# Optimization experiments

Measured on AMD Instinct MI355X. Metric: run time of the kernel, lower is better.

Reference implementation:

```python
import jax, jax.numpy as jnp
import numpy as np

N, C, S = 262144, 256, 16
BN_EPS = 1e-5


def setup_inputs() -> dict:
    key = jax.random.key(0)
    ks = jax.random.split(key, 8)
    x = jax.random.normal(ks[0], (N, C), dtype=jnp.float32)
    # strictly increasing cumulative offsets ending at N (guarantees nonzero counts)
    rng = np.random.default_rng(0)
    cuts = np.sort(rng.choice(np.arange(1, N), size=S - 1, replace=False))
    o = jnp.asarray(np.concatenate([cuts, [N]]), dtype=jnp.int64)
    # linear2_: Linear(C, C) (+ReLU, no BN in this branch)
    W2 = jax.random.normal(ks[1], (C, C), dtype=jnp.float32) / np.sqrt(C)
    b2 = jax.random.normal(ks[2], (C,), dtype=jnp.float32) * 0.01
    # linear1_: Linear(2C, C) + BatchNorm1d(C) + ReLU
    W1 = jax.random.normal(ks[3], (2 * C, C), dtype=jnp.float32) / np.sqrt(2 * C)
    b1 = jax.random.normal(ks[4], (C,), dtype=jnp.float32) * 0.01
    gamma = jnp.ones((C,), dtype=jnp.float32)
    beta = jnp.zeros((C,), dtype=jnp.float32)
    run_mean = jax.random.normal(ks[5], (C,), dtype=jnp.float32) * 0.01
    run_var = jnp.ones((C,), dtype=jnp.float32)
    return {"x": x, "o": o, "W2": W2, "b2": b2, "W1": W1, "b1": b1,
            "gamma": gamma, "beta": beta, "run_mean": run_mean, "run_var": run_var}


def reference(x, o, W2, b2, W1, b1, gamma, beta, run_mean, run_var):
    n, c = x.shape
    num_seg = o.shape[0]
    # segment id of each point: first offset strictly greater than index
    seg_ids = jnp.searchsorted(o, jnp.arange(n), side="right")  # [N]
    counts = jnp.diff(o, prepend=0).astype(x.dtype)             # [S]
    sums = jax.ops.segment_sum(x, seg_ids, num_segments=num_seg)  # [S, C]
    means = sums / counts[:, None]
    # linear2_ on per-segment mean, broadcast back to points
    h = jax.nn.relu(means @ W2 + b2)                            # [S, C]
    xc = jnp.concatenate([x, h[seg_ids]], axis=1)               # [N, 2C]
    # linear1_: Linear + BatchNorm1d (inference, running stats) + ReLU
    y = xc @ W1 + b1
    y = (y - run_mean) * jax.lax.rsqrt(run_var + BN_EPS) * gamma + beta
    return jax.nn.relu(y)
```

## Files before the change

### kernel.cpp

```cpp
#include <hip/hip_runtime.h>

#define C_DIM 256
#define S_SEG 16

typedef __attribute__((ext_vector_type(8))) short bf16x8;
typedef __attribute__((ext_vector_type(4))) float f32x4;

__device__ __forceinline__ short f2bf(float f) {
    unsigned u = __builtin_bit_cast(unsigned, f);
    u += 0x7FFF + ((u >> 16) & 1);
    return (short)(u >> 16);
}

__device__ __forceinline__ int o_get(const int* __restrict__ o_raw, int i) {
    return (o_raw[1] == 0) ? o_raw[2 * i] : o_raw[i];
}

__global__ __launch_bounds__(256) void k1_segsum(const float* __restrict__ x,
                                                 const int* __restrict__ o_raw,
                                                 float* __restrict__ sums) {
    __shared__ int o_s[S_SEG];
    __shared__ float4 partv[256];
    __shared__ int pseg[256];
    int t = threadIdx.x;
    if (t < S_SEG) o_s[t] = o_get(o_raw, t);
    __syncthreads();

    int rsub = t >> 6, cg = t & 63;
    int row0 = blockIdx.x * 256 + rsub * 64;
    const float4* xv = (const float4*)x;

    int cur = 0;
#pragma unroll
    for (int j = 0; j < S_SEG; ++j) cur += (row0 >= o_s[j]);
    int next = o_s[cur];

    float4 acc = make_float4(0.f, 0.f, 0.f, 0.f);
    for (int i = 0; i < 64; ++i) {
        int row = row0 + i;
        if (row >= next) {
            atomicAdd(&sums[cur * C_DIM + cg * 4 + 0], acc.x);
            atomicAdd(&sums[cur * C_DIM + cg * 4 + 1], acc.y);
            atomicAdd(&sums[cur * C_DIM + cg * 4 + 2], acc.z);
            atomicAdd(&sums[cur * C_DIM + cg * 4 + 3], acc.w);
            acc = make_float4(0.f, 0.f, 0.f, 0.f);
            do { cur++; next = o_s[cur]; } while (row >= next);
        }
        float4 v = xv[row * 64 + cg];
        acc.x += v.x; acc.y += v.y; acc.z += v.z; acc.w += v.w;
    }
    partv[t] = acc;
    pseg[t] = cur;
    __syncthreads();

    if (t < 64) {
        float4 a = partv[t];
        int s = pseg[t];
        for (int i = 1; i < 4; ++i) {
            int idx = i * 64 + t;
            int s2 = pseg[idx];
            float4 a2 = partv[idx];
            if (s2 == s) {
                a.x += a2.x; a.y += a2.y; a.z += a2.z; a.w += a2.w;
            } else {
                atomicAdd(&sums[s * C_DIM + t * 4 + 0], a.x);
                atomicAdd(&sums[s * C_DIM + t * 4 + 1], a.y);
                atomicAdd(&sums[s * C_DIM + t * 4 + 2], a.z);
                atomicAdd(&sums[s * C_DIM + t * 4 + 3], a.w);
                s = s2; a = a2;
            }
        }
        atomicAdd(&sums[s * C_DIM + t * 4 + 0], a.x);
        atomicAdd(&sums[s * C_DIM + t * 4 + 1], a.y);
        atomicAdd(&sums[s * C_DIM + t * 4 + 2], a.z);
        atomicAdd(&sums[s * C_DIM + t * 4 + 3], a.w);
    }
}

__global__ __launch_bounds__(256) void k2_small(const float* __restrict__ sums,
                                                const int* __restrict__ o_raw,
                                                const float* __restrict__ W2,
                                                const float* __restrict__ b2,
                                                const float* __restrict__ W1,
                                                const float* __restrict__ b1,
                                                const float* __restrict__ gamma,
                                                const float* __restrict__ beta,
                                                const float* __restrict__ rmean,
                                                const float* __restrict__ rvar,
                                                float* __restrict__ Cseg,
                                                short* __restrict__ W1s) {
    int t = threadIdx.x;
    int blk = blockIdx.x;
    if (blk < S_SEG) {
        __shared__ float mean_s[C_DIM];
        __shared__ float h_s[C_DIM];
        int s = blk;
        int lo = (s == 0) ? 0 : o_get(o_raw, s - 1);
        float inv = 1.0f / (float)(o_get(o_raw, s) - lo);
        mean_s[t] = sums[s * C_DIM + t] * inv;
        __syncthreads();
        float acc = b2[t];
#pragma unroll 4
        for (int k = 0; k < C_DIM; ++k) acc = fmaf(mean_s[k], W2[k * C_DIM + t], acc);
        h_s[t] = fmaxf(acc, 0.0f);
        __syncthreads();
        float acc2 = 0.f;
#pragma unroll 4
        for (int k = 0; k < C_DIM; ++k) acc2 = fmaf(h_s[k], W1[(C_DIM + k) * C_DIM + t], acc2);
        float sc = gamma[t] * rsqrtf(rvar[t] + 1e-5f);
        Cseg[s * C_DIM + t] = (b1[t] + acc2 - rmean[t]) * sc + beta[t];
    } else {
        int base = (blk - S_SEG) * 8192;
        for (int i = 0; i < 32; ++i) {
            int idx = base + i * 256 + t;
            int k = idx >> 8, c = idx & 255;
            float sc = gamma[c] * rsqrtf(rvar[c] + 1e-5f);
            float v = W1[k * C_DIM + c] * sc;
            int kb2 = k >> 5, q = (k >> 3) & 3, j = k & 7, nsub = c >> 4, r = c & 15;
            int off = ((kb2 * 16 + nsub) * 64 + q * 16 + r) * 8 + j;
            W1s[off] = f2bf(v);
        }
    }
}

__global__ __launch_bounds__(256) void k3_gemm(const float* __restrict__ x,
                                               const short* __restrict__ W1s,
                                               const float* __restrict__ Cseg,
                                               const int* __restrict__ o_raw,
                                               float* __restrict__ out) {
    __shared__ __align__(16) short As[2][4 * 2 * 64 * 8];
    __shared__ int o_s[S_SEG];

    int t = threadIdx.x;
    int wave = t >> 6, lane = t & 63;
    int q = lane >> 4, r = lane & 15;
    int wc = wave;
    int m0 = (int)(gridDim.x - 1 - blockIdx.x) * 64;

    if (t < S_SEG) o_s[t] = o_get(o_raw, t);

    f32x4 acc[4][4];
#pragma unroll
    for (int mt = 0; mt < 4; ++mt)
#pragma unroll
        for (int nt = 0; nt < 4; ++nt)
            acc[mt][nt] = (f32x4){0.f, 0.f, 0.f, 0.f};

    const float4* xv = (const float4*)x;
    int arow = t >> 3;
    int akc = t & 7;
    int kt_w = akc >> 2, q_w = akc & 3;
    int mt0 = arow >> 4, r0 = arow & 15;
    int slot0 = (mt0 * 2 + kt_w) * 64 + q_w * 16 + (r0 ^ q_w);
    int row1 = 32 + arow, mt1 = row1 >> 4, r1 = row1 & 15;
    int slot1 = (mt1 * 2 + kt_w) * 64 + q_w * 16 + (r1 ^ q_w);
    long gbase0 = (long)(m0 + arow) * 64 + akc * 2;
    long gbase1 = (long)(m0 + 32 + arow) * 64 + akc * 2;

    float4 c00, c01, c10, c11;
    c00 = xv[gbase0]; c01 = xv[gbase0 + 1];
    c10 = xv[gbase1]; c11 = xv[gbase1 + 1];
    {
        bf16x8 w0, w1;
        w0[0] = f2bf(c00.x); w0[1] = f2bf(c00.y); w0[2] = f2bf(c00.z); w0[3] = f2bf(c00.w);
        w0[4] = f2bf(c01.x); w0[5] = f2bf(c01.y); w0[6] = f2bf(c01.z); w0[7] = f2bf(c01.w);
        *(bf16x8*)&As[0][slot0 * 8] = w0;
        w1[0] = f2bf(c10.x); w1[1] = f2bf(c10.y); w1[2] = f2bf(c10.z); w1[3] = f2bf(c10.w);
        w1[4] = f2bf(c11.x); w1[5] = f2bf(c11.y); w1[6] = f2bf(c11.z); w1[7] = f2bf(c11.w);
        *(bf16x8*)&As[0][slot1 * 8] = w1;
    }
    __syncthreads();

    for (int kb = 0; kb < 4; ++kb) {
        if (kb < 3) {
            long o = (long)(kb + 1) * 16;
            c00 = xv[gbase0 + o]; c01 = xv[gbase0 + o + 1];
            c10 = xv[gbase1 + o]; c11 = xv[gbase1 + o + 1];
        }
        const short* Ab = As[kb & 1];
#pragma unroll
        for (int kt = 0; kt < 2; ++kt) {
            bf16x8 a[4], b[4];
#pragma unroll
            for (int mt = 0; mt < 4; ++mt)
                a[mt] = *(const bf16x8*)&Ab[((mt * 2 + kt) * 64 + q * 16 + (r ^ q)) * 8];
#pragma unroll
            for (int nt = 0; nt < 4; ++nt)
                b[nt] = *(const bf16x8*)&W1s[(((kb * 2 + kt) * 16 + wc * 4 + nt) * 64 + lane) * 8];
#pragma unroll
            for (int mt = 0; mt < 4; ++mt)
#pragma unroll
                for (int nt = 0; nt < 4; ++nt)
                    acc[mt][nt] = __builtin_amdgcn_mfma_f32_16x16x32_bf16(a[mt], b[nt], acc[mt][nt], 0, 0, 0);
        }
        if (kb < 3) {
            short* Aw = As[(kb + 1) & 1];
            bf16x8 w0, w1;
            w0[0] = f2bf(c00.x); w0[1] = f2bf(c00.y); w0[2] = f2bf(c00.z); w0[3] = f2bf(c00.w);
            w0[4] = f2bf(c01.x); w0[5] = f2bf(c01.y); w0[6] = f2bf(c01.z); w0[7] = f2bf(c01.w);
            *(bf16x8*)&Aw[slot0 * 8] = w0;
            w1[0] = f2bf(c10.x); w1[1] = f2bf(c10.y); w1[2] = f2bf(c10.z); w1[3] = f2bf(c10.w);
            w1[4] = f2bf(c11.x); w1[5] = f2bf(c11.y); w1[6] = f2bf(c11.z); w1[7] = f2bf(c11.w);
            *(bf16x8*)&Aw[slot1 * 8] = w1;
            __syncthreads();
        }
    }

#pragma unroll
    for (int mt = 0; mt < 4; ++mt) {
#pragma unroll
        for (int i = 0; i < 4; ++i) {
            int row = m0 + mt * 16 + q * 4 + i;
            int s = 0;
#pragma unroll
            for (int j = 0; j < S_SEG; ++j) s += (row >= o_s[j]);
#pragma unroll
            for (int nt = 0; nt < 4; ++nt) {
                int col = wc * 64 + nt * 16 + r;
                float v = acc[mt][nt][i] + Cseg[s * C_DIM + col];
                __builtin_nontemporal_store(fmaxf(v, 0.0f), &out[(long)row * C_DIM + col]);
            }
        }
    }
}

extern "C" void kernel_launch(void* const* d_in, const int* in_sizes, int n_in,
                              void* d_out, int out_size, void* d_ws, size_t ws_size,
                              hipStream_t stream) {
    const float* x     = (const float*)d_in[0];
    const int*   o     = (const int*)d_in[1];
    const float* W2    = (const float*)d_in[2];
    const float* b2    = (const float*)d_in[3];
    const float* W1    = (const float*)d_in[4];
    const float* b1    = (const float*)d_in[5];
    const float* gamma = (const float*)d_in[6];
    const float* beta  = (const float*)d_in[7];
    const float* rmean = (const float*)d_in[8];
    const float* rvar  = (const float*)d_in[9];
    float* out = (float*)d_out;

    float* sums = (float*)d_ws;
    float* Cseg = (float*)((char*)d_ws + 16384);
    short* W1s  = (short*)((char*)d_ws + 65536);

    hipMemsetAsync(d_ws, 0, 16384, stream);
    k1_segsum<<<1024, 256, 0, stream>>>(x, o, sums);
    k2_small<<<24, 256, 0, stream>>>(sums, o, W2, b2, W1, b1, gamma, beta, rmean, rvar, Cseg, W1s);
    k3_gemm<<<4096, 256, 0, stream>>>(x, W1s, Cseg, o, out);
}
```

Measured before the change: 602.8 us.

## Emit bf16 copy of x in segsum and stream it directly into MFMA GEMM

The segment-sum kernel now also converts x to bf16 and writes it to workspace. A new GEMM kernel then loads bf16 A fragments straight from global memory into registers, double-buffered across K blocks, with no LDS staging or fp32-to-bf16 conversion. Output is written with nontemporal stores. This adds a 128 MB write in k1 but halves the x read in k3 and drops LDS traffic. The old path is kept as a fallback when the workspace is too small.

```diff
diff --git a/kernel.cpp b/kernel.cpp
--- a/kernel.cpp
+++ b/kernel.cpp
@@ -2,8 +2,10 @@
 
 #define C_DIM 256
 #define S_SEG 16
+#define N_PTS 262144
 
 typedef __attribute__((ext_vector_type(8))) short bf16x8;
+typedef __attribute__((ext_vector_type(4))) short bf16x4;
 typedef __attribute__((ext_vector_type(4))) float f32x4;
 
 __device__ __forceinline__ short f2bf(float f) {
@@ -16,9 +18,11 @@
     return (o_raw[1] == 0) ? o_raw[2 * i] : o_raw[i];
 }
 
+template <bool WRITE_XB>
 __global__ __launch_bounds__(256) void k1_segsum(const float* __restrict__ x,
                                                  const int* __restrict__ o_raw,
-                                                 float* __restrict__ sums) {
+                                                 float* __restrict__ sums,
+                                                 short* __restrict__ xb) {
     __shared__ int o_s[S_SEG];
     __shared__ float4 partv[256];
     __shared__ int pseg[256];
@@ -47,6 +51,11 @@
             do { cur++; next = o_s[cur]; } while (row >= next);
         }
         float4 v = xv[row * 64 + cg];
+        if (WRITE_XB) {
+            bf16x4 w;
+            w[0] = f2bf(v.x); w[1] = f2bf(v.y); w[2] = f2bf(v.z); w[3] = f2bf(v.w);
+            *(bf16x4*)&xb[(row << 8) + (cg << 2)] = w;
+        }
         acc.x += v.x; acc.y += v.y; acc.z += v.z; acc.w += v.w;
     }
     partv[t] = acc;
@@ -123,11 +132,90 @@
     }
 }
 
-__global__ __launch_bounds__(256) void k3_gemm(const float* __restrict__ x,
+#define K3_LOAD(A, B, kb)                                                          \
+    {                                                                              \
+        _Pragma("unroll")                                                          \
+        for (int kt = 0; kt < 2; ++kt) {                                           \
+            _Pragma("unroll")                                                      \
+            for (int mt = 0; mt < 4; ++mt)                                         \
+                A[kt][mt] = *(const bf16x8*)&xb[abase[mt] + (kb) * 64 + kt * 32];  \
+            _Pragma("unroll")                                                      \
+            for (int nt = 0; nt < 4; ++nt)                                         \
+                B[kt][nt] = *(const bf16x8*)&W1s[(kb) * 16384 + kt * 8192 + bb + nt * 512]; \
+        }                                                                          \
+    }
+
+#define K3_MFMA(A, B)                                                              \
+    {                                                                              \
+        _Pragma("unroll")                                                          \
+        for (int kt = 0; kt < 2; ++kt)                                             \
+            _Pragma("unroll")                                                      \
+            for (int mt = 0; mt < 4; ++mt)                                         \
+                _Pragma("unroll")                                                  \
+                for (int nt = 0; nt < 4; ++nt)                                     \
+                    acc[mt][nt] = __builtin_amdgcn_mfma_f32_16x16x32_bf16(          \
+                        A[kt][mt], B[kt][nt], acc[mt][nt], 0, 0, 0);               \
+    }
+
+__global__ __launch_bounds__(256) void k3_gemm(const short* __restrict__ xb,
                                                const short* __restrict__ W1s,
                                                const float* __restrict__ Cseg,
                                                const int* __restrict__ o_raw,
                                                float* __restrict__ out) {
+    int t = threadIdx.x;
+    int wave = t >> 6, lane = t & 63;
+    int q = lane >> 4, r = lane & 15;
+    int m0 = (int)blockIdx.x * 64;
+
+    f32x4 acc[4][4];
+#pragma unroll
+    for (int mt = 0; mt < 4; ++mt)
+#pragma unroll
+        for (int nt = 0; nt < 4; ++nt)
+            acc[mt][nt] = (f32x4){0.f, 0.f, 0.f, 0.f};
+
+    int abase[4];
+#pragma unroll
+    for (int mt = 0; mt < 4; ++mt) abase[mt] = ((m0 + mt * 16 + r) << 8) + (q << 3);
+    int bb = (wave << 11) + (lane << 3);
+
+    bf16x8 a0[2][4], b0[2][4], a1[2][4], b1[2][4];
+    K3_LOAD(a0, b0, 0)
+    K3_LOAD(a1, b1, 1)
+    K3_MFMA(a0, b0)
+    K3_LOAD(a0, b0, 2)
+    K3_MFMA(a1, b1)
+    K3_LOAD(a1, b1, 3)
+    K3_MFMA(a0, b0)
+    K3_MFMA(a1, b1)
+
+    int ov[S_SEG];
+#pragma unroll
+    for (int j = 0; j < S_SEG; ++j) ov[j] = o_get(o_raw, j);
+
+#pragma unroll
+    for (int mt = 0; mt < 4; ++mt) {
+#pragma unroll
+        for (int i = 0; i < 4; ++i) {
+            int row = m0 + mt * 16 + q * 4 + i;
+            int s = 0;
+#pragma unroll
+            for (int j = 0; j < S_SEG; ++j) s += (row >= ov[j]);
+#pragma unroll
+            for (int nt = 0; nt < 4; ++nt) {
+                int col = wave * 64 + nt * 16 + r;
+                float v = acc[mt][nt][i] + Cseg[s * C_DIM + col];
+                __builtin_nontemporal_store(fmaxf(v, 0.0f), &out[(long)row * C_DIM + col]);
+            }
+        }
+    }
+}
+
+__global__ __launch_bounds__(256) void k3_gemm_f32lds(const float* __restrict__ x,
+                                                      const short* __restrict__ W1s,
+                                                      const float* __restrict__ Cseg,
+                                                      const int* __restrict__ o_raw,
+                                                      float* __restrict__ out) {
     __shared__ __align__(16) short As[2][4 * 2 * 64 * 8];
     __shared__ int o_s[S_SEG];
 
@@ -239,12 +327,23 @@
     const float* rvar  = (const float*)d_in[9];
     float* out = (float*)d_out;
 
+    const int N = N_PTS;
+
     float* sums = (float*)d_ws;
     float* Cseg = (float*)((char*)d_ws + 16384);
     short* W1s  = (short*)((char*)d_ws + 65536);
+    size_t xb_off = (size_t)1 << 20;
+    short* xb   = (short*)((char*)d_ws + xb_off);
+    size_t need = xb_off + (size_t)N * C_DIM * 2;
 
     hipMemsetAsync(d_ws, 0, 16384, stream);
-    k1_segsum<<<1024, 256, 0, stream>>>(x, o, sums);
-    k2_small<<<24, 256, 0, stream>>>(sums, o, W2, b2, W1, b1, gamma, beta, rmean, rvar, Cseg, W1s);
-    k3_gemm<<<4096, 256, 0, stream>>>(x, W1s, Cseg, o, out);
-}
+    if (ws_size >= need) {
+        k1_segsum<true><<<N / 256, 256, 0, stream>>>(x, o, sums, xb);
+        k2_small<<<24, 256, 0, stream>>>(sums, o, W2, b2, W1, b1, gamma, beta, rmean, rvar, Cseg, W1s);
+        k3_gemm<<<N / 64, 256, 0, stream>>>(xb, W1s, Cseg, o, out);
+    } else {
+        k1_segsum<false><<<N / 256, 256, 0, stream>>>(x, o, sums, nullptr);
+        k2_small<<<24, 256, 0, stream>>>(sums, o, W2, b2, W1, b1, gamma, beta, rmean, rvar, Cseg, W1s);
+        k3_gemm_f32lds<<<N / 64, 256, 0, stream>>>(x, W1s, Cseg, o, out);
+    }
+}
```

New measurement: 645.0 us. +7.0%, slower.
